# Optimization experiments

Hardware: AMD Instinct MI355X
Metric: run time of the kernel (lower is better)

## Reference

```python
import jax, jax.numpy as jnp
import numpy as np

NUM_CLASSES = 1024
DEPTH = 10  # num_edges; complete binary tree over 2**DEPTH leaves
BATCH = 4096


def _build_tree_buffers(C=NUM_CLASSES, D=DEPTH):
    """Replicates HierarchicalLLLoss.__init__ for a complete binary hierarchy.
    onehot_num[i, :, j] = indicator of leaves under leaf i's ancestor j levels up.
    onehot_den[i, :, j] = indicator one level further up; last column is all-ones.
    weights[i, j]       = edge weight at level j (deterministic exp decay).
    """
    ids = np.arange(C)
    onehot_num = np.zeros((C, C, D), dtype=np.float32)
    onehot_den = np.zeros((C, C, D), dtype=np.float32)
    for j in range(D):
        blk = 2 ** j
        onehot_num[:, :, j] = (ids[:, None] // blk == ids[None, :] // blk)
        if j < D - 1:
            blk2 = 2 ** (j + 1)
            onehot_den[:, :, j] = (ids[:, None] // blk2 == ids[None, :] // blk2)
    onehot_den[:, :, D - 1] = 1.0
    weights = np.tile(np.exp(-0.5 * np.arange(D, dtype=np.float32))[None, :], (C, 1))
    return onehot_num, onehot_den, weights


def setup_inputs() -> dict:
    key = jax.random.key(0)
    k1, k2 = jax.random.split(key)
    # class probabilities: uniform then normalized per row
    logits = jax.random.uniform(k1, (BATCH, NUM_CLASSES), dtype=jnp.float32) + 1e-3
    inputs = logits / jnp.sum(logits, axis=1, keepdims=True)
    target = jax.random.randint(k2, (BATCH,), 0, NUM_CLASSES, dtype=jnp.int64)
    onehot_num, onehot_den, weights = _build_tree_buffers()
    return {
        "inputs": inputs,
        "target": target,
        "onehot_num": jnp.asarray(onehot_num),
        "onehot_den": jnp.asarray(onehot_den),
        "weights": jnp.asarray(weights),
    }


def reference(inputs, target, onehot_num, onehot_den, weights):
    # gather per-sample onehot trees: [B, C, E]
    oh_num = onehot_num[target]
    oh_den = onehot_den[target]
    num = jnp.einsum('bc,bce->be', inputs, oh_num)
    den = jnp.einsum('bc,bce->be', inputs, oh_den)
    idx = num != 0
    safe_num = jnp.where(idx, num, 1.0)
    safe_den = jnp.where(idx, den, 1.0)
    # where num==0, torch leaves num (==0) untouched
    val = jnp.where(idx, -jnp.log(safe_num / safe_den), num)
    # torch.flip along dim=1 is a no-op under the subsequent sum over dim=1
    per_sample = jnp.sum(weights[target] * val, axis=1)  # [B]
    return jnp.mean(per_sample)
```

## Files before the change

### kernel.cpp

```cpp
#include <hip/hip_runtime.h>

#define BATCH 4096
#define NCLS  1024
#define DEPTH 10
#define WPB   8
#define NBLOCKS (BATCH / WPB)

__global__ __launch_bounds__(WPB * 64) void hll_per_block(
    const float* __restrict__ inputs,
    const int*   __restrict__ target,
    const float* __restrict__ weights,
    float*       __restrict__ partials)
{
    const int wave = threadIdx.x >> 6;
    const int lane = threadIdx.x & 63;
    const int b = blockIdx.x * WPB + wave;

    const float4* row4 = reinterpret_cast<const float4*>(inputs + (size_t)b * NCLS);

    float4 x0 = row4[lane];
    float4 x1 = row4[64 + lane];
    float4 x2 = row4[128 + lane];
    float4 x3 = row4[192 + lane];

    const int t  = __builtin_amdgcn_readfirstlane(target[b]);
    const int ct = t >> 2;
    const int st = ct >> 6;
    const int lt = ct & 63;
    const int r  = t & 3;

    const float4 xt = (st == 0) ? x0 : (st == 1) ? x1 : (st == 2) ? x2 : x3;

    const float cs0 = x0.x + x0.y + x0.z + x0.w;
    const float cs1 = x1.x + x1.y + x1.z + x1.w;
    const float cs2 = x2.x + x2.y + x2.z + x2.w;
    const float cs3 = x3.x + x3.y + x3.z + x3.w;
    const float cst = (st == 0) ? cs0 : (st == 1) ? cs1 : (st == 2) ? cs2 : cs3;

    float S[DEPTH + 1];
    S[0] = (r == 0) ? xt.x : (r == 1) ? xt.y : (r == 2) ? xt.z : xt.w;
    S[1] = (r < 2) ? (xt.x + xt.y) : (xt.z + xt.w);
    S[2] = cst;

    float a = cst;
    #pragma unroll
    for (int k = 0; k < 6; ++k) {
        a += __shfl_xor(a, 1 << k, 64);
        S[3 + k] = a;
    }

    float p = (st < 2) ? (cs0 + cs1) : (cs2 + cs3);
    float o = (st < 2) ? (cs2 + cs3) : (cs0 + cs1);
    #pragma unroll
    for (int k = 0; k < 6; ++k) {
        p += __shfl_xor(p, 1 << k, 64);
        o += __shfl_xor(o, 1 << k, 64);
    }
    S[9]  = p;
    S[10] = p + o;

    float acc = 0.0f;
    #pragma unroll
    for (int j = 0; j < DEPTH; ++j) {
        const float num = S[j];
        const float den = S[j + 1];
        const float val = (num != 0.0f) ? -__logf(num / den) : num;
        acc += weights[j] * val;
    }

    __shared__ float wsum[WPB];
    if (lane == lt) wsum[wave] = acc;
    __syncthreads();
    if (threadIdx.x == 0) {
        float sum = 0.0f;
        #pragma unroll
        for (int i = 0; i < WPB; ++i) sum += wsum[i];
        partials[blockIdx.x] = sum;
    }
}

__global__ __launch_bounds__(64) void hll_reduce(
    const float* __restrict__ partials,
    float*       __restrict__ out)
{
    const int lane = threadIdx.x;
    const float4* p4 = reinterpret_cast<const float4*>(partials);
    float s = 0.0f;
    #pragma unroll
    for (int i = 0; i < NBLOCKS / 256; ++i) {
        float4 v = p4[lane + i * 64];
        s += v.x + v.y + v.z + v.w;
    }
    #pragma unroll
    for (int k = 0; k < 6; ++k)
        s += __shfl_xor(s, 1 << k, 64);
    if (lane == 0) out[0] = s * (1.0f / (float)BATCH);
}

extern "C" void kernel_launch(void* const* d_in, const int* in_sizes, int n_in,
                              void* d_out, int out_size, void* d_ws, size_t ws_size,
                              hipStream_t stream) {
    const float* inputs  = (const float*)d_in[0];
    const int*   target  = (const int*)d_in[1];
    const float* weights = (const float*)d_in[4];

    float* partials = (float*)d_ws;
    float* out      = (float*)d_out;

    hll_per_block<<<NBLOCKS, WPB * 64, 0, stream>>>(inputs, target, weights, partials);
    hll_reduce<<<1, 64, 0, stream>>>(partials, out);
}
```

Before: 11.28 us.

## Fuse final reduction via fixed-point atomics and last-block completion counter

Replaces the second reduce kernel with per-block 64-bit fixed-point atomic adds into a workspace accumulator plus an atomic block counter. The last block to finish converts the sum to float and writes the mean. This removes one kernel launch and the partials round trip, but adds a hipMemsetAsync each call and atomic contention on a single address. The counter increment also encodes high bits of the old sum, which is an odd trick that could corrupt the count if the sum grows large.

Measured after the change: 25.48 us. +125.9%, slower.

```diff
diff --git a/kernel.cpp b/kernel.cpp
--- a/kernel.cpp
+++ b/kernel.cpp
@@ -6,11 +6,13 @@
 #define WPB   8
 #define NBLOCKS (BATCH / WPB)
 
-__global__ __launch_bounds__(WPB * 64) void hll_per_block(
+__global__ __launch_bounds__(WPB * 64) void hll_fused(
     const float* __restrict__ inputs,
     const int*   __restrict__ target,
     const float* __restrict__ weights,
-    float*       __restrict__ partials)
+    unsigned long long* __restrict__ sum_fx,
+    unsigned int*       __restrict__ count,
+    float*              __restrict__ out)
 {
     const int wave = threadIdx.x >> 6;
     const int lane = threadIdx.x & 63;
@@ -71,30 +73,26 @@
     __shared__ float wsum[WPB];
     if (lane == lt) wsum[wave] = acc;
     __syncthreads();
+
     if (threadIdx.x == 0) {
-        float sum = 0.0f;
+        float psum = 0.0f;
         #pragma unroll
-        for (int i = 0; i < WPB; ++i) sum += wsum[i];
-        partials[blockIdx.x] = sum;
+        for (int i = 0; i < WPB; ++i) psum += wsum[i];
+
+        const unsigned long long q =
+            (unsigned long long)(long long)(psum * 4294967296.0);
+
+        const unsigned long long oldsum = atomicAdd(sum_fx, q);
+        const unsigned int inc = 1u | (unsigned int)(oldsum >> 62);
+        const unsigned int oldc = atomicAdd(count, inc);
+
+        if (oldc == NBLOCKS - 1) {
+            const unsigned long long tot = atomicAdd(sum_fx, 0ULL);
+            const double v = (double)(long long)tot *
+                             (1.0 / 4294967296.0) * (1.0 / (double)BATCH);
+            out[0] = (float)v;
+        }
     }
-}
-
-__global__ __launch_bounds__(64) void hll_reduce(
-    const float* __restrict__ partials,
-    float*       __restrict__ out)
-{
-    const int lane = threadIdx.x;
-    const float4* p4 = reinterpret_cast<const float4*>(partials);
-    float s = 0.0f;
-    #pragma unroll
-    for (int i = 0; i < NBLOCKS / 256; ++i) {
-        float4 v = p4[lane + i * 64];
-        s += v.x + v.y + v.z + v.w;
-    }
-    #pragma unroll
-    for (int k = 0; k < 6; ++k)
-        s += __shfl_xor(s, 1 << k, 64);
-    if (lane == 0) out[0] = s * (1.0f / (float)BATCH);
 }
 
 extern "C" void kernel_launch(void* const* d_in, const int* in_sizes, int n_in,
@@ -104,9 +102,12 @@
     const int*   target  = (const int*)d_in[1];
     const float* weights = (const float*)d_in[4];
 
-    float* partials = (float*)d_ws;
-    float* out      = (float*)d_out;
+    unsigned long long* sum_fx = (unsigned long long*)d_ws;
+    unsigned int*       count  = (unsigned int*)((char*)d_ws + 8);
+    float*              out    = (float*)d_out;
 
-    hll_per_block<<<NBLOCKS, WPB * 64, 0, stream>>>(inputs, target, weights, partials);
-    hll_reduce<<<1, 64, 0, stream>>>(partials, out);
+    hipMemsetAsync(d_ws, 0, 16, stream);
+
+    hll_fused<<<NBLOCKS, WPB * 64, 0, stream>>>(inputs, target, weights,
+                                                sum_fx, count, out);
 }
```
